# Optimization experiments

Measured on AMD Instinct MI355X. Metric: run time of the kernel, lower is better.

Reference implementation:

```python
import jax, jax.numpy as jnp
import numpy as np

B, N, C = 8, 512, 256
HID_E = 32          # edge_pred hidden width
FILTERS = (64, 64, 64)
OUT = 2


def setup_inputs() -> dict:
    key = jax.random.key(0)
    ks = jax.random.split(key, 12)
    s = 0.05
    inp = {
        "x": jax.random.normal(ks[0], (B, N, C), jnp.float32),
        "A": jax.random.uniform(ks[1], (B, N, N), jnp.float32),
        "mask": jnp.ones((B, N), jnp.float32),
        # edge predictor: Linear(2C,32) -> ReLU -> Linear(32,1)
        "ew1": jax.random.normal(ks[2], (2 * C, HID_E), jnp.float32) * s,
        "eb1": jnp.zeros((HID_E,), jnp.float32),
        "ew2": jax.random.normal(ks[3], (HID_E, 1), jnp.float32) * s,
        "eb2": jnp.zeros((1,), jnp.float32),
        # GraphConv stack: Linear(in*n_relations, f) per layer (n_relations=2)
        "gw0": jax.random.normal(ks[4], (2 * C, FILTERS[0]), jnp.float32) * s,
        "gb0": jnp.zeros((FILTERS[0],), jnp.float32),
        "gw1": jax.random.normal(ks[5], (2 * FILTERS[0], FILTERS[1]), jnp.float32) * s,
        "gb1": jnp.zeros((FILTERS[1],), jnp.float32),
        "gw2": jax.random.normal(ks[6], (2 * FILTERS[1], FILTERS[2]), jnp.float32) * s,
        "gb2": jnp.zeros((FILTERS[2],), jnp.float32),
        # final classifier (dropout is identity in eval)
        "fcw": jax.random.normal(ks[7], (FILTERS[2], OUT), jnp.float32) * s,
        "fcb": jnp.zeros((OUT,), jnp.float32),
    }
    return inp


def _laplacian(A):
    # A_hat = A + I ; L = D^-1/2 A_hat D^-1/2 with D from row-sums (dim 1)
    n = A.shape[-1]
    A_hat = A + jnp.eye(n, dtype=A.dtype)
    D = (A_hat.sum(axis=1) + 1e-5) ** -0.5  # [B,N]
    return D[:, :, None] * A_hat * D[:, None, :]


def reference(x, A, mask, ew1, eb1, ew2, eb2, gw0, gb0, gw1, gb1, gw2, gb2, fcw, fcb):
    b, n, c = x.shape
    # edge MLP over all node pairs; first layer split so we never build [B,N,N,2C]
    wa, wb = ew1[:c], ew1[c:]
    xa = x @ wa  # [B,N,32] contribution of node i
    xb = x @ wb  # [B,N,32] contribution of node j
    h = jax.nn.relu(xa[:, :, None, :] + xb[:, None, :, :] + eb1)  # [B,N,N,32]
    e = (h @ ew2)[..., 0] + eb2[0]  # e[b,i,j] = edge_pred([x_i, x_j])
    # symmetrized score: exp(0.5 * (f(i,j) + f(j,i)))
    y = jnp.exp(0.5 * (e + jnp.swapaxes(e, 1, 2)))
    triu = jnp.triu(jnp.ones((n, n), bool), 1)
    valid = (mask[:, :, None] > 0) & (mask[:, None, :] > 0)
    A_pred = jnp.where(triu[None] & valid, y, 0.0)
    A_pred = A_pred + jnp.swapaxes(A_pred, 1, 2)

    # multi-relation GCN stack (relations: input A, predicted A_pred)
    L0 = _laplacian(A)
    L1 = _laplacian(A_pred)
    m = mask[:, :, None]
    h0 = x
    for W, bias in ((gw0, gb0), (gw1, gb1), (gw2, gb2)):
        xh = jnp.concatenate([L0 @ h0, L1 @ h0], axis=-1)  # [B,N,2*f_in]
        h0 = jax.nn.relu((xh @ W + bias) * m)
    g = h0.max(axis=1)  # [B, filters[-1]] global max pool over nodes
    return g @ fcw + fcb  # [B, OUT]
```

## Files before the change

### kernel.cpp

```cpp
#include <hip/hip_runtime.h>
#include <hip/hip_bf16.h>
#include <math.h>

#define NB 8
#define NN 512
#define NC 256
#define HID 32

typedef __attribute__((ext_vector_type(8))) short short8;
typedef __attribute__((ext_vector_type(4))) float float4v;
typedef unsigned short ushort_t;

__device__ __forceinline__ ushort_t f2bf(float x) {
    unsigned u = __float_as_uint(x);
    return (ushort_t)((u + 0x7fffu + ((u >> 16) & 1u)) >> 16);
}
__device__ __forceinline__ float bf2f(ushort_t h) {
    return __uint_as_float(((unsigned)h) << 16);
}

__global__ __launch_bounds__(256) void front_gemms(
    const float* __restrict__ x, const float* __restrict__ ew1,
    const float* __restrict__ eb1, const float* __restrict__ gw0,
    float* __restrict__ xab, ushort_t* __restrict__ T0,
    float* __restrict__ dsum, unsigned* __restrict__ gmax, int* __restrict__ done)
{
    __shared__ __align__(16) union {
        struct { float sX[2][32][17]; float sW[2][32][68]; } a;
        struct { float sH[2][32][17]; float sW[2][32][132]; ushort_t sTh[128][24]; } b;
    } u;
    int t = threadIdx.x;

    if (blockIdx.x < 256) {
        if (blockIdx.x < 32) dsum[blockIdx.x * 256 + t] = 0.f;
        if (blockIdx.x == 32) {
            gmax[t] = 0u; gmax[t + 256] = 0u;
            if (t < NB) done[t] = 0;
        }
        int r0 = blockIdx.x * 16;
        int tx = t & 15, ty = t >> 4;
        int xk = (t & 15) * 2, xr = t >> 4;
        int c4 = (t & 15) * 4;
        int whalf = c4 >> 5, wcc = c4 & 31;
        float acc[4] = {0.f, 0.f, 0.f, 0.f};

        float2 rx = *(const float2*)(x + (size_t)(r0 + xr) * NC + xk);
        float4 rw0 = *(const float4*)(ew1 + (size_t)(whalf * NC + xr) * HID + wcc);
        float4 rw1 = *(const float4*)(ew1 + (size_t)(whalf * NC + xr + 16) * HID + wcc);

        for (int k0 = 0; k0 < NC; k0 += 32) {
            int cur = (k0 >> 5) & 1;
            u.a.sX[cur][xk][xr] = rx.x; u.a.sX[cur][xk + 1][xr] = rx.y;
            *(float4*)&u.a.sW[cur][xr][c4] = rw0;
            *(float4*)&u.a.sW[cur][xr + 16][c4] = rw1;
            if (k0 + 32 < NC) {
                rx  = *(const float2*)(x + (size_t)(r0 + xr) * NC + k0 + 32 + xk);
                rw0 = *(const float4*)(ew1 + (size_t)(whalf * NC + k0 + 32 + xr) * HID + wcc);
                rw1 = *(const float4*)(ew1 + (size_t)(whalf * NC + k0 + 32 + xr + 16) * HID + wcc);
            }
            __syncthreads();
#pragma unroll
            for (int k = 0; k < 32; ++k) {
                float a = u.a.sX[cur][k][ty];
                float4 w = *(const float4*)&u.a.sW[cur][k][tx * 4];
                acc[0] = fmaf(a, w.x, acc[0]); acc[1] = fmaf(a, w.y, acc[1]);
                acc[2] = fmaf(a, w.z, acc[2]); acc[3] = fmaf(a, w.w, acc[3]);
            }
        }
        int oc4 = tx * 4;
        float4 o; o.x = acc[0]; o.y = acc[1]; o.z = acc[2]; o.w = acc[3];
        if (oc4 >= 32) {
            o.x += eb1[oc4 - 32]; o.y += eb1[oc4 - 31];
            o.z += eb1[oc4 - 30]; o.w += eb1[oc4 - 29];
        }
        *(float4*)&xab[(size_t)(r0 + ty) * 64 + oc4] = o;
    } else {
        int r0 = (blockIdx.x - 256) * 16;
        int tx = t & 31, ty = t >> 5;
        int xk = (t & 15) * 2, xr = t >> 4;
        int c4w = (t & 31) * 4;
        int whalf = c4w >> 6, wcc = c4w & 63;
        int wk = t >> 5;
        float acc0[4] = {0.f, 0.f, 0.f, 0.f};
        float acc1[4] = {0.f, 0.f, 0.f, 0.f};

        float2 rx = *(const float2*)(x + (size_t)(r0 + xr) * NC + xk);
        float4 rw[4];
#pragma unroll
        for (int rr = 0; rr < 4; ++rr)
            rw[rr] = *(const float4*)(gw0 + (size_t)(whalf * NC + wk + rr * 8) * 64 + wcc);

        for (int k0 = 0; k0 < NC; k0 += 32) {
            int cur = (k0 >> 5) & 1;
            u.b.sH[cur][xk][xr] = rx.x; u.b.sH[cur][xk + 1][xr] = rx.y;
#pragma unroll
            for (int rr = 0; rr < 4; ++rr)
                *(float4*)&u.b.sW[cur][wk + rr * 8][c4w] = rw[rr];
            if (k0 + 32 < NC) {
                rx = *(const float2*)(x + (size_t)(r0 + xr) * NC + k0 + 32 + xk);
#pragma unroll
                for (int rr = 0; rr < 4; ++rr)
                    rw[rr] = *(const float4*)(gw0 + (size_t)(whalf * NC + k0 + 32 + wk + rr * 8) * 64 + wcc);
            }
            __syncthreads();
#pragma unroll
            for (int k = 0; k < 32; ++k) {
                float a0 = u.b.sH[cur][k][ty * 2];
                float a1 = u.b.sH[cur][k][ty * 2 + 1];
                float4 w = *(const float4*)&u.b.sW[cur][k][tx * 4];
                acc0[0] = fmaf(a0, w.x, acc0[0]); acc0[1] = fmaf(a0, w.y, acc0[1]);
                acc0[2] = fmaf(a0, w.z, acc0[2]); acc0[3] = fmaf(a0, w.w, acc0[3]);
                acc1[0] = fmaf(a1, w.x, acc1[0]); acc1[1] = fmaf(a1, w.y, acc1[1]);
                acc1[2] = fmaf(a1, w.z, acc1[2]); acc1[3] = fmaf(a1, w.w, acc1[3]);
            }
        }
        __syncthreads();
        int c4 = tx * 4;
#pragma unroll
        for (int r = 0; r < 2; ++r) {
            int rl = ty * 2 + r;
            float* ap = (r == 0) ? acc0 : acc1;
#pragma unroll
            for (int n = 0; n < 4; ++n)
                u.b.sTh[c4 + n][rl] = f2bf(ap[n]);
        }
        __syncthreads();
        {
            int c = t & 127, half = t >> 7;
            int bb = r0 >> 9, ibase = r0 & (NN - 1);
            ushort_t* dst = T0 + ((size_t)(bb * 128 + c)) * NN + ibase + half * 8;
            *(short8*)dst = *(const short8*)&u.b.sTh[c][half * 8];
        }
    }
}

__global__ __launch_bounds__(256) void edge_scores(
    const float* __restrict__ xab, const float* __restrict__ ew2,
    const float* __restrict__ eb2, const float* __restrict__ mask,
    const float* __restrict__ A, ushort_t* __restrict__ Ah,
    ushort_t* __restrict__ APh, float* __restrict__ dsum)
{
    __shared__ __align__(16) float sI[32][68], sJ[32][68];
    __shared__ float sV[32][33];
    int b = blockIdx.z;
    int p = blockIdx.x;
    int X = 0;
    while ((X + 1) * 16 - ((X + 1) * X) / 2 <= p) ++X;
    int Y = X + (p - (X * 16 - (X * (X - 1)) / 2));
    int i0 = X * 32, j0 = Y * 32;
    int t = threadIdx.x;
    int tj = t & 31;

    float4 rW[8];
#pragma unroll
    for (int k4 = 0; k4 < 8; ++k4) rW[k4] = *(const float4*)(ew2 + k4 * 4);
    float eb2v = eb2[0];

    {
        int c4 = (t & 15) * 4;
#pragma unroll
        for (int rr = 0; rr < 2; ++rr) {
            int r = (t >> 4) + rr * 16;
            float4 vi = *(const float4*)(xab + ((size_t)(b * NN + i0 + r)) * 64 + c4);
            float4 vj = *(const float4*)(xab + ((size_t)(b * NN + j0 + r)) * 64 + c4);
            *(float4*)&sI[r][c4] = vi;
            *(float4*)&sJ[r][c4] = vj;
        }
    }
    __syncthreads();

    float rJlo[32], rJhi[32];
#pragma unroll
    for (int k4 = 0; k4 < 8; ++k4) {
        float4 a4 = *(const float4*)&sJ[tj][k4 * 4];
        float4 b4 = *(const float4*)&sJ[tj][32 + k4 * 4];
        rJlo[k4 * 4 + 0] = a4.x; rJlo[k4 * 4 + 1] = a4.y;
        rJlo[k4 * 4 + 2] = a4.z; rJlo[k4 * 4 + 3] = a4.w;
        rJhi[k4 * 4 + 0] = b4.x; rJhi[k4 * 4 + 1] = b4.y;
        rJhi[k4 * 4 + 2] = b4.z; rJhi[k4 * 4 + 3] = b4.w;
    }
    float mj = mask[b * NN + j0 + tj];

#pragma unroll
    for (int pz = 0; pz < 4; ++pz) {
        int ti = (t >> 5) + pz * 8;
        float sij = 0.f, sji = 0.f;
#pragma unroll
        for (int k4 = 0; k4 < 8; ++k4) {
            float4 ia = *(const float4*)&sI[ti][k4 * 4];
            float4 ib = *(const float4*)&sI[ti][32 + k4 * 4];
            float4 wv = rW[k4];
            sij = fmaf(fmaxf(ia.x + rJhi[k4 * 4 + 0], 0.f), wv.x, sij);
            sji = fmaf(fmaxf(rJlo[k4 * 4 + 0] + ib.x, 0.f), wv.x, sji);
            sij = fmaf(fmaxf(ia.y + rJhi[k4 * 4 + 1], 0.f), wv.y, sij);
            sji = fmaf(fmaxf(rJlo[k4 * 4 + 1] + ib.y, 0.f), wv.y, sji);
            sij = fmaf(fmaxf(ia.z + rJhi[k4 * 4 + 2], 0.f), wv.z, sij);
            sji = fmaf(fmaxf(rJlo[k4 * 4 + 2] + ib.z, 0.f), wv.z, sji);
            sij = fmaf(fmaxf(ia.w + rJhi[k4 * 4 + 3], 0.f), wv.w, sij);
            sji = fmaf(fmaxf(rJlo[k4 * 4 + 3] + ib.w, 0.f), wv.w, sji);
        }
        int i = i0 + ti, j = j0 + tj;
        bool ok = (i != j) && (mask[b * NN + i] > 0.f) && (mj > 0.f);
        sV[ti][tj] = ok ? expf(0.5f * (sij + sji) + eb2v) : 0.f;
    }
    __syncthreads();
#pragma unroll
    for (int pz = 0; pz < 4; ++pz) {
        int r = (t >> 5) + pz * 8, c = t & 31;
        size_t o1 = ((size_t)(b * NN + i0 + r)) * NN + j0 + c;
        size_t o2 = ((size_t)(b * NN + j0 + r)) * NN + i0 + c;
        APh[o1] = f2bf(sV[r][c]);
        APh[o2] = f2bf(sV[c][r]);
    }
    if (t < 32) {
        float s = 0.f;
#pragma unroll
        for (int r = 0; r < 32; ++r) s += sV[r][t];
        atomicAdd(&dsum[(NB * NN) + b * NN + j0 + t], s);
    } else if (t < 64 && X != Y) {
        int c = t - 32;
        float s = 0.f;
#pragma unroll
        for (int j = 0; j < 32; ++j) s += sV[c][j];
        atomicAdd(&dsum[(NB * NN) + b * NN + i0 + c], s);
    }
    if (p < 128) {
        const float* Ar = A + ((size_t)b * NN + 4 * p) * NN;
        ushort_t* Hr = Ah + ((size_t)b * NN + 4 * p) * NN;
        float s0 = 0.f, s1 = 0.f;
#pragma unroll
        for (int rr = 0; rr < 4; ++rr) {
            float a0 = Ar[(size_t)rr * NN + t];
            float a1 = Ar[(size_t)rr * NN + t + 256];
            Hr[(size_t)rr * NN + t] = f2bf(a0);
            Hr[(size_t)rr * NN + t + 256] = f2bf(a1);
            s0 += a0; s1 += a1;
        }
        atomicAdd(&dsum[b * NN + t], s0);
        atomicAdd(&dsum[b * NN + t + 256], s1);
    }
}

__global__ __launch_bounds__(256) void fused_layer(
    const ushort_t* __restrict__ Ah, const ushort_t* __restrict__ APh,
    const ushort_t* __restrict__ Pa, const ushort_t* __restrict__ Pb,
    ushort_t* __restrict__ Qa, ushort_t* __restrict__ Qb,
    const float* __restrict__ dsum, const float* __restrict__ gb,
    const float* __restrict__ mask, const float* __restrict__ gwN,
    unsigned* __restrict__ gmax, int* __restrict__ done,
    const float* __restrict__ fcw, const float* __restrict__ fcb,
    float* __restrict__ out, int dualP, int mode, int scaleP)
{
    __shared__ union {
        struct {
            ushort_t sA[2][2][16][72];
            ushort_t sP1[2][64][72];
            ushort_t sP2[2][64][72];
        } a;
        struct { ushort_t sWT[128][40]; } b;
    } u;
    __shared__ float sRed[2][32][17];
    __shared__ float sH16[16][36];
    __shared__ float sD[2][16];
    __shared__ __align__(16) float sDj[2][NN];
    __shared__ int lastFlag;

    int t = threadIdx.x;
    int b = blockIdx.z, ch = blockIdx.y, i0 = blockIdx.x * 16;
    int lane = t & 63, w = t >> 6;
    int quad = lane >> 4, m16 = lane & 15;
    int lap = w >> 1, cg = w & 1;

    if (scaleP) {
#pragma unroll
        for (int s = 0; s < 4; ++s) {
            int idx = t + s * 256;
            int lp = idx >> 9, j = idx & (NN - 1);
            sDj[lp][j] = rsqrtf(dsum[lp * (NB * NN) + b * NN + j] + 1.0f + 1e-5f);
        }
    }

    int sa_arr = t >> 7, sa_id = t & 127;
    int sa_r = sa_id >> 3, sa_q = sa_id & 7;
    const ushort_t* sa_src = (sa_arr ? APh : Ah)
        + ((size_t)(b * NN + i0 + sa_r)) * NN + sa_q * 8;
    int pl0 = t >> 3, pq = t & 7;
    size_t poff0 = ((size_t)(b * 128 + ch * 32 + pl0)) * NN + pq * 8;
    size_t poff1 = ((size_t)(b * 128 + 64 + ch * 32 + pl0)) * NN + pq * 8;

    int gi = b * NN + i0 + m16;
    float dspre = dsum[lap * (NB * NN) + gi];
    int cbase = cg * 16 + quad * 4;
    size_t pvbase = ((size_t)(b * 128 + lap * 64 + ch * 32 + cbase)) * NN + i0 + m16;
    ushort_t pvA[4], pvB[4];
#pragma unroll
    for (int r = 0; r < 4; ++r) {
        pvA[r] = Pa[pvbase + (size_t)r * NN];
        pvB[r] = dualP ? Pb[pvbase + (size_t)r * NN] : (ushort_t)0;
    }

    float4v acc = {0.f, 0.f, 0.f, 0.f};

    short8 rA   = *(const short8*)(sa_src);
    short8 rP1a = *(const short8*)(Pa + poff0);
    short8 rP1b = *(const short8*)(Pa + poff1);
    short8 rP2a = rP1a, rP2b = rP1b;
    if (dualP) {
        rP2a = *(const short8*)(Pb + poff0);
        rP2b = *(const short8*)(Pb + poff1);
    }
    __syncthreads();

    for (int k0 = 0; k0 < NN; k0 += 64) {
        int cur = (k0 >> 6) & 1;
        *(short8*)&u.a.sA[cur][sa_arr][sa_r][sa_q * 8] = rA;
        if (scaleP) {
            float4v d0a = *(const float4v*)&sDj[0][k0 + pq * 8];
            float4v d0b = *(const float4v*)&sDj[0][k0 + pq * 8 + 4];
            float4v d1a = *(const float4v*)&sDj[1][k0 + pq * 8];
            float4v d1b = *(const float4v*)&sDj[1][k0 + pq * 8 + 4];
            short8 w0, w1;
#pragma unroll
            for (int e = 0; e < 4; ++e) {
                w0[e]     = (short)f2bf(bf2f((ushort_t)rP1a[e])     * d0a[e]);
                w0[e + 4] = (short)f2bf(bf2f((ushort_t)rP1a[e + 4]) * d0b[e]);
                w1[e]     = (short)f2bf(bf2f((ushort_t)rP1b[e])     * d1a[e]);
                w1[e + 4] = (short)f2bf(bf2f((ushort_t)rP1b[e + 4]) * d1b[e]);
            }
            *(short8*)&u.a.sP1[cur][pl0][pq * 8] = w0;
            *(short8*)&u.a.sP1[cur][32 + pl0][pq * 8] = w1;
        } else {
            *(short8*)&u.a.sP1[cur][pl0][pq * 8] = rP1a;
            *(short8*)&u.a.sP1[cur][32 + pl0][pq * 8] = rP1b;
            if (dualP) {
                *(short8*)&u.a.sP2[cur][pl0][pq * 8] = rP2a;
                *(short8*)&u.a.sP2[cur][32 + pl0][pq * 8] = rP2b;
            }
        }
        if (k0 + 64 < NN) {
            rA   = *(const short8*)(sa_src + k0 + 64);
            rP1a = *(const short8*)(Pa + poff0 + k0 + 64);
            rP1b = *(const short8*)(Pa + poff1 + k0 + 64);
            if (dualP) {
                rP2a = *(const short8*)(Pb + poff0 + k0 + 64);
                rP2b = *(const short8*)(Pb + poff1 + k0 + 64);
            }
        }
        __syncthreads();
#pragma unroll
        for (int kh = 0; kh < 2; ++kh) {
            int ko = kh * 32 + quad * 8;
            short8 av = *(const short8*)&u.a.sA[cur][lap][m16][ko];
            short8 p1 = *(const short8*)&u.a.sP1[cur][w * 16 + m16][ko];
            acc = __builtin_amdgcn_mfma_f32_16x16x32_bf16(p1, av, acc, 0, 0, 0);
            if (dualP) {
                short8 p2 = *(const short8*)&u.a.sP2[cur][w * 16 + m16][ko];
                acc = __builtin_amdgcn_mfma_f32_16x16x32_bf16(p2, av, acc, 0, 0, 0);
            }
        }
    }
    float d = rsqrtf(dspre + 1.0f + 1e-5f);
    if (cg == 0 && quad == 0) sD[lap][m16] = d;
#pragma unroll
    for (int r = 0; r < 4; ++r) {
        int c32 = cbase + r;
        float pv = bf2f(pvA[r]);
        if (dualP) pv += bf2f(pvB[r]);
        if (scaleP) pv *= d;
        sRed[lap][c32][m16] = d * (acc[r] + pv);
    }
    __syncthreads();
#pragma unroll
    for (int s = 0; s < 2; ++s) {
        int idx = t + s * 256;
        int c32 = idx & 31, i = idx >> 5;
        float mv = mask[b * NN + i0 + i];
        float v = (sRed[0][c32][i] + sRed[1][c32][i] + gb[ch * 32 + c32]) * mv;
        sH16[i][c32] = fmaxf(v, 0.f);
    }
    __syncthreads();

    if (mode == 0) {
#pragma unroll
        for (int kk = 0; kk < 8; ++kk) {
            int chunk = t + kk * 256;
            int c = chunk & 127;
            int k = (chunk >> 7) * 2;
            int base = (c < 64) ? (ch * 32) : (64 + ch * 32);
            int gc = c & 63;
            float f0 = gwN[(size_t)(base + k) * 64 + gc];
            float f1 = gwN[(size_t)(base + k + 1) * 64 + gc];
            unsigned pk = (unsigned)f2bf(f0) | ((unsigned)f2bf(f1) << 16);
            *(unsigned*)&u.b.sWT[c][k] = pk;
        }
        __syncthreads();
        float4 h0 = *(const float4*)&sH16[m16][quad * 8];
        float4 h1 = *(const float4*)&sH16[m16][quad * 8 + 4];
        short8 bfv;
        bfv[0] = f2bf(h0.x); bfv[1] = f2bf(h0.y); bfv[2] = f2bf(h0.z); bfv[3] = f2bf(h0.w);
        bfv[4] = f2bf(h1.x); bfv[5] = f2bf(h1.y); bfv[6] = f2bf(h1.z); bfv[7] = f2bf(h1.w);
        ushort_t* Q = ch ? Qb : Qa;
#pragma unroll
        for (int s2 = 0; s2 < 2; ++s2) {
            int ctile = w * 2 + s2;
            short8 af = *(const short8*)&u.b.sWT[ctile * 16 + m16][quad * 8];
            float4v dacc = {0.f, 0.f, 0.f, 0.f};
            dacc = __builtin_amdgcn_mfma_f32_16x16x32_bf16(af, bfv, dacc, 0, 0, 0);
            float dsc = sD[(ctile >= 4) ? 1 : 0][m16];
#pragma unroll
            for (int r = 0; r < 4; ++r) {
                int c = ctile * 16 + quad * 4 + r;
                Q[((size_t)(b * 128 + c)) * NN + i0 + m16] = f2bf(dsc * dacc[r]);
            }
        }
    } else {
        if (t < 32) {
            float mx = 0.f;
#pragma unroll
            for (int r = 0; r < 16; ++r) mx = fmaxf(mx, sH16[r][t]);
            atomicMax(&gmax[b * 64 + ch * 32 + t], __float_as_uint(mx));
        }
        __syncthreads();
        if (t == 0) {
            __threadfence();
            int old = atomicAdd(&done[b], 1);
            lastFlag = (old == 63);
        }
        __syncthreads();
        if (lastFlag) {
            if (t < 64) {
                unsigned ub = __hip_atomic_load(&gmax[b * 64 + t],
                                                __ATOMIC_RELAXED,
                                                __HIP_MEMORY_SCOPE_AGENT);
                ((float*)sRed)[t] = __uint_as_float(ub);
            }
            __syncthreads();
            if (t < 2) {
                float a2 = fcb[t];
#pragma unroll
                for (int k = 0; k < 64; ++k)
                    a2 = fmaf(((float*)sRed)[k], fcw[k * 2 + t], a2);
                out[b * 2 + t] = a2;
            }
        }
    }
}

extern "C" void kernel_launch(void* const* d_in, const int* in_sizes, int n_in,
                              void* d_out, int out_size, void* d_ws, size_t ws_size,
                              hipStream_t stream)
{
    const float* x    = (const float*)d_in[0];
    const float* A    = (const float*)d_in[1];
    const float* mask = (const float*)d_in[2];
    const float* ew1  = (const float*)d_in[3];
    const float* eb1  = (const float*)d_in[4];
    const float* ew2  = (const float*)d_in[5];
    const float* eb2  = (const float*)d_in[6];
    const float* gw0  = (const float*)d_in[7];
    const float* gb0  = (const float*)d_in[8];
    const float* gw1  = (const float*)d_in[9];
    const float* gb1  = (const float*)d_in[10];
    const float* gw2  = (const float*)d_in[11];
    const float* gb2  = (const float*)d_in[12];
    const float* fcw  = (const float*)d_in[13];
    const float* fcb  = (const float*)d_in[14];
    float* out = (float*)d_out;
    char* ws = (char*)d_ws;

    const size_t NEL = (size_t)NB * NN * NN;
    const size_t PSL = (size_t)NB * 128 * NN;
    float*    xab  = (float*)ws;                   ws += 262144 * 4;
    ushort_t* APh  = (ushort_t*)ws;                ws += NEL * 2;
    ushort_t* Ahs  = (ushort_t*)ws;                ws += NEL * 2;
    float*    dsum = (float*)ws;                   ws += 8192 * 4;
    ushort_t* PT_A = (ushort_t*)ws;                ws += PSL * 2;
    ushort_t* PB1a = (ushort_t*)ws;                ws += PSL * 2;
    ushort_t* PB1b = (ushort_t*)ws;                ws += PSL * 2;
    ushort_t* PB2a = (ushort_t*)ws;                ws += PSL * 2;
    ushort_t* PB2b = (ushort_t*)ws;                ws += PSL * 2;
    unsigned* gmax = (unsigned*)ws;                ws += 512 * 4;
    int*      done = (int*)ws;                     ws += 64 * 4;

    front_gemms<<<512, 256, 0, stream>>>(x, ew1, eb1, gw0, xab, PT_A,
                                         dsum, gmax, done);
    edge_scores<<<dim3(136, 1, NB), 256, 0, stream>>>(xab, ew2, eb2, mask,
                                                      A, Ahs, APh, dsum);

    fused_layer<<<dim3(32, 2, NB), 256, 0, stream>>>(
        Ahs, APh, PT_A, PT_A, PB1a, PB1b, dsum, gb0, mask, gw1,
        gmax, done, fcw, fcb, out, 0, 0, 1);
    fused_layer<<<dim3(32, 2, NB), 256, 0, stream>>>(
        Ahs, APh, PB1a, PB1b, PB2a, PB2b, dsum, gb1, mask, gw2,
        gmax, done, fcw, fcb, out, 1, 0, 0);
    fused_layer<<<dim3(32, 2, NB), 256, 0, stream>>>(
        Ahs, APh, PB2a, PB2b, PB2a, PB2b, dsum, gb2, mask, gw2,
        gmax, done, fcw, fcb, out, 1, 1, 0);
}
```

Baseline: 156.2 us.

## Load MFMA operands directly from global memory instead of LDS staging

```diff
diff --git a/kernel.cpp b/kernel.cpp
--- a/kernel.cpp
+++ b/kernel.cpp
@@ -251,14 +251,7 @@
     const float* __restrict__ fcw, const float* __restrict__ fcb,
     float* __restrict__ out, int dualP, int mode, int scaleP)
 {
-    __shared__ union {
-        struct {
-            ushort_t sA[2][2][16][72];
-            ushort_t sP1[2][64][72];
-            ushort_t sP2[2][64][72];
-        } a;
-        struct { ushort_t sWT[128][40]; } b;
-    } u;
+    __shared__ ushort_t sWT[128][40];
     __shared__ float sRed[2][32][17];
     __shared__ float sH16[16][36];
     __shared__ float sD[2][16];
@@ -278,15 +271,14 @@
             int lp = idx >> 9, j = idx & (NN - 1);
             sDj[lp][j] = rsqrtf(dsum[lp * (NB * NN) + b * NN + j] + 1.0f + 1e-5f);
         }
-    }
-
-    int sa_arr = t >> 7, sa_id = t & 127;
-    int sa_r = sa_id >> 3, sa_q = sa_id & 7;
-    const ushort_t* sa_src = (sa_arr ? APh : Ah)
-        + ((size_t)(b * NN + i0 + sa_r)) * NN + sa_q * 8;
-    int pl0 = t >> 3, pq = t & 7;
-    size_t poff0 = ((size_t)(b * 128 + ch * 32 + pl0)) * NN + pq * 8;
-    size_t poff1 = ((size_t)(b * 128 + 64 + ch * 32 + pl0)) * NN + pq * 8;
+        __syncthreads();
+    }
+
+    const ushort_t* Abase = (lap ? APh : Ah)
+        + ((size_t)(b * NN + i0 + m16)) * NN + quad * 8;
+    int prow = b * 128 + lap * 64 + ch * 32 + cg * 16 + m16;
+    const ushort_t* P1base = Pa + (size_t)prow * NN + quad * 8;
+    const ushort_t* P2base = Pb + (size_t)prow * NN + quad * 8;
 
     int gi = b * NN + i0 + m16;
     float dspre = dsum[lap * (NB * NN) + gi];
@@ -301,64 +293,32 @@
 
     float4v acc = {0.f, 0.f, 0.f, 0.f};
 
-    short8 rA   = *(const short8*)(sa_src);
-    short8 rP1a = *(const short8*)(Pa + poff0);
-    short8 rP1b = *(const short8*)(Pa + poff1);
-    short8 rP2a = rP1a, rP2b = rP1b;
-    if (dualP) {
-        rP2a = *(const short8*)(Pb + poff0);
-        rP2b = *(const short8*)(Pb + poff1);
-    }
-    __syncthreads();
-
+#pragma unroll
     for (int k0 = 0; k0 < NN; k0 += 64) {
-        int cur = (k0 >> 6) & 1;
-        *(short8*)&u.a.sA[cur][sa_arr][sa_r][sa_q * 8] = rA;
-        if (scaleP) {
-            float4v d0a = *(const float4v*)&sDj[0][k0 + pq * 8];
-            float4v d0b = *(const float4v*)&sDj[0][k0 + pq * 8 + 4];
-            float4v d1a = *(const float4v*)&sDj[1][k0 + pq * 8];
-            float4v d1b = *(const float4v*)&sDj[1][k0 + pq * 8 + 4];
-            short8 w0, w1;
-#pragma unroll
-            for (int e = 0; e < 4; ++e) {
-                w0[e]     = (short)f2bf(bf2f((ushort_t)rP1a[e])     * d0a[e]);
-                w0[e + 4] = (short)f2bf(bf2f((ushort_t)rP1a[e + 4]) * d0b[e]);
-                w1[e]     = (short)f2bf(bf2f((ushort_t)rP1b[e])     * d1a[e]);
-                w1[e + 4] = (short)f2bf(bf2f((ushort_t)rP1b[e + 4]) * d1b[e]);
-            }
-            *(short8*)&u.a.sP1[cur][pl0][pq * 8] = w0;
-            *(short8*)&u.a.sP1[cur][32 + pl0][pq * 8] = w1;
-        } else {
-            *(short8*)&u.a.sP1[cur][pl0][pq * 8] = rP1a;
-            *(short8*)&u.a.sP1[cur][32 + pl0][pq * 8] = rP1b;
-            if (dualP) {
-                *(short8*)&u.a.sP2[cur][pl0][pq * 8] = rP2a;
-                *(short8*)&u.a.sP2[cur][32 + pl0][pq * 8] = rP2b;
-            }
-        }
-        if (k0 + 64 < NN) {
-            rA   = *(const short8*)(sa_src + k0 + 64);
-            rP1a = *(const short8*)(Pa + poff0 + k0 + 64);
-            rP1b = *(const short8*)(Pa + poff1 + k0 + 64);
-            if (dualP) {
-                rP2a = *(const short8*)(Pb + poff0 + k0 + 64);
-                rP2b = *(const short8*)(Pb + poff1 + k0 + 64);
-            }
-        }
-        __syncthreads();
 #pragma unroll
         for (int kh = 0; kh < 2; ++kh) {
-            int ko = kh * 32 + quad * 8;
-            short8 av = *(const short8*)&u.a.sA[cur][lap][m16][ko];
-            short8 p1 = *(const short8*)&u.a.sP1[cur][w * 16 + m16][ko];
+            int ko = k0 + kh * 32;
+            short8 av = *(const short8*)(Abase + ko);
+            short8 p1 = *(const short8*)(P1base + ko);
+            if (scaleP) {
+                float4v dja = *(const float4v*)&sDj[lap][ko + quad * 8];
+                float4v djb = *(const float4v*)&sDj[lap][ko + quad * 8 + 4];
+                short8 w0;
+#pragma unroll
+                for (int e = 0; e < 4; ++e) {
+                    w0[e]     = (short)f2bf(bf2f((ushort_t)p1[e])     * dja[e]);
+                    w0[e + 4] = (short)f2bf(bf2f((ushort_t)p1[e + 4]) * djb[e]);
+                }
+                p1 = w0;
+            }
             acc = __builtin_amdgcn_mfma_f32_16x16x32_bf16(p1, av, acc, 0, 0, 0);
             if (dualP) {
-                short8 p2 = *(const short8*)&u.a.sP2[cur][w * 16 + m16][ko];
+                short8 p2 = *(const short8*)(P2base + ko);
                 acc = __builtin_amdgcn_mfma_f32_16x16x32_bf16(p2, av, acc, 0, 0, 0);
             }
         }
     }
+
     float d = rsqrtf(dspre + 1.0f + 1e-5f);
     if (cg == 0 && quad == 0) sD[lap][m16] = d;
 #pragma unroll
@@ -391,7 +351,7 @@
             float f0 = gwN[(size_t)(base + k) * 64 + gc];
             float f1 = gwN[(size_t)(base + k + 1) * 64 + gc];
             unsigned pk = (unsigned)f2bf(f0) | ((unsigned)f2bf(f1) << 16);
-            *(unsigned*)&u.b.sWT[c][k] = pk;
+            *(unsigned*)&sWT[c][k] = pk;
         }
         __syncthreads();
         float4 h0 = *(const float4*)&sH16[m16][quad * 8];
@@ -403,7 +363,7 @@
 #pragma unroll
         for (int s2 = 0; s2 < 2; ++s2) {
             int ctile = w * 2 + s2;
-            short8 af = *(const short8*)&u.b.sWT[ctile * 16 + m16][quad * 8];
+            short8 af = *(const short8*)&sWT[ctile * 16 + m16][quad * 8];
             float4v dacc = {0.f, 0.f, 0.f, 0.f};
             dacc = __builtin_amdgcn_mfma_f32_16x16x32_bf16(af, bfv, dacc, 0, 0, 0);
             float dsc = sD[(ctile >= 4) ? 1 : 0][m16];
```

Measured after the change: 173.2 us. 1.11x slower.
